# Optimization experiments

Measured on AMD Instinct MI355X. Metric: run time of the kernel, lower is better.

## Reference

```python
import jax, jax.numpy as jnp
import numpy as np

N, E, IN_DIM, HID, OUT, H = 50000, 800000, 128, 96, 96, 4
C1, C2 = HID // H, OUT // H
EPS = 1e-5

def _lin(key, out_f, in_f):
    kw, kb = jax.random.split(key)
    s = 1.0 / np.sqrt(in_f)
    W = jax.random.uniform(kw, (out_f, in_f), jnp.float32, -s, s)
    b = jax.random.uniform(kb, (out_f,), jnp.float32, -s, s)
    return W, b

def setup_inputs() -> dict:
    key = jax.random.key(0)
    ks = jax.random.split(key, 16)
    x = jax.random.normal(ks[0], (N, IN_DIM), jnp.float32)
    edge_index = jax.random.randint(ks[1], (2, E), 0, N, jnp.int64)
    Wq1, bq1 = _lin(ks[2], HID, IN_DIM)
    Wk1, bk1 = _lin(ks[3], HID, IN_DIM)
    Wv1, bv1 = _lin(ks[4], HID, IN_DIM)
    Ws1, bs1 = _lin(ks[5], HID, IN_DIM)
    Wb1 = _lin(ks[6], 1, 3 * HID)[0]
    Wq2, bq2 = _lin(ks[7], OUT, HID)
    Wk2, bk2 = _lin(ks[8], OUT, HID)
    Wv2, bv2 = _lin(ks[9], OUT, HID)
    Ws2, bs2 = _lin(ks[10], OUT, HID)
    Wb2 = _lin(ks[11], 1, 3 * OUT)[0]
    gamma = jnp.ones((OUT,), jnp.float32)
    beta = jnp.zeros((OUT,), jnp.float32)
    return dict(x=x, edge_index=edge_index, Wq1=Wq1, bq1=bq1, Wk1=Wk1, bk1=bk1,
                Wv1=Wv1, bv1=bv1, Ws1=Ws1, bs1=bs1, Wb1=Wb1,
                Wq2=Wq2, bq2=bq2, Wk2=Wk2, bk2=bk2, Wv2=Wv2, bv2=bv2,
                Ws2=Ws2, bs2=bs2, Wb2=Wb2, gamma=gamma, beta=beta)

def transformer_conv(x, src, dst, Wq, bq, Wk, bk, Wv, bv, Ws, bs, Wb, heads, ch):
    n = x.shape[0]
    q = (x @ Wq.T + bq).reshape(n, heads, ch)
    k = (x @ Wk.T + bk).reshape(n, heads, ch)
    v = (x @ Wv.T + bv).reshape(n, heads, ch)
    # per-edge attention logits [E, H]
    alpha = jnp.einsum('ehc,ehc->eh', q[dst], k[src]) / jnp.sqrt(jnp.float32(ch))
    amax = jax.ops.segment_max(alpha, dst, num_segments=n)
    a = jnp.exp(alpha - amax[dst])
    denom = jax.ops.segment_sum(a, dst, num_segments=n)
    a = a / denom[dst]
    msg = v[src] * a[:, :, None]                       # [E, H, C]
    out = jax.ops.segment_sum(msg, dst, num_segments=n).reshape(n, heads * ch)
    x_r = x @ Ws.T + bs                                # root/skip transform
    g = jax.nn.sigmoid(jnp.concatenate([out, x_r, out - x_r], -1) @ Wb.T)
    return g * x_r + (1.0 - g) * out

def reference(x, edge_index, Wq1, bq1, Wk1, bk1, Wv1, bv1, Ws1, bs1, Wb1,
              Wq2, bq2, Wk2, bk2, Wv2, bv2, Ws2, bs2, Wb2, gamma, beta):
    src, dst = edge_index[0], edge_index[1]
    h = transformer_conv(x, src, dst, Wq1, bq1, Wk1, bk1, Wv1, bv1, Ws1, bs1, Wb1, H, C1)
    h = jax.nn.gelu(h, approximate=False)
    h = transformer_conv(h, src, dst, Wq2, bq2, Wk2, bk2, Wv2, bv2, Ws2, bs2, Wb2, H, C2)
    mu = jnp.mean(h, axis=-1, keepdims=True)
    var = jnp.mean(jnp.square(h - mu), axis=-1, keepdims=True)
    return (h - mu) / jnp.sqrt(var + EPS) * gamma + beta
```

## Files before the change

### kernel.cpp

```cpp
#include <hip/hip_runtime.h>
#include <hip/hip_bf16.h>
#include <hip/hip_fp16.h>
#include <math.h>

constexpr int NN = 50000;
constexpr int EE = 800000;
constexpr int SCAN_NB = (NN + 255) / 256;

typedef short v8s __attribute__((ext_vector_type(8)));
typedef float v4f __attribute__((ext_vector_type(4)));

__device__ __forceinline__ short f2b(float f){
  __hip_bfloat16 h = __float2bfloat16(f);
  return *reinterpret_cast<short*>(&h);
}
__device__ __forceinline__ __half2 u2h2(unsigned int u){
  union { unsigned int u; __half2 h; } c; c.u = u; return c.h;
}

__global__ void hist_kernel(const int* __restrict__ ei, int* __restrict__ deg){
  int e = blockIdx.x * blockDim.x + threadIdx.x;
  if (e < EE) atomicAdd(&deg[ei[EE + e]], 1);
}

__global__ __launch_bounds__(256) void partial_sum_kernel(const int* __restrict__ deg,
                                                          int* __restrict__ psum){
  int b = blockIdx.x, tid = threadIdx.x, lane = tid & 63, wv = tid >> 6;
  int i = b * 256 + tid;
  int v = (i < NN) ? deg[i] : 0;
  #pragma unroll
  for (int m = 1; m < 64; m <<= 1) v += __shfl_xor(v, m);
  __shared__ int ws[4];
  if (lane == 0) ws[wv] = v;
  __syncthreads();
  if (tid == 0) psum[b] = ws[0] + ws[1] + ws[2] + ws[3];
}

__global__ __launch_bounds__(256) void scan_partials_kernel(int* __restrict__ psum){
  int tid = threadIdx.x, lane = tid & 63, wv = tid >> 6;
  int own = (tid < SCAN_NB) ? psum[tid] : 0;
  int v = own;
  #pragma unroll
  for (int off = 1; off < 64; off <<= 1){
    int t = __shfl_up(v, off);
    if (lane >= off) v += t;
  }
  __shared__ int ws[4];
  if (lane == 63) ws[wv] = v;
  __syncthreads();
  int add = 0;
  #pragma unroll
  for (int w = 0; w < 4; w++) if (w < wv) add += ws[w];
  if (tid < SCAN_NB) psum[tid] = v + add - own;
}

__global__ __launch_bounds__(256) void final_scan_kernel(const int* __restrict__ deg,
                                                         const int* __restrict__ psum,
                                                         int* __restrict__ row_ptr,
                                                         int* __restrict__ cursor){
  int b = blockIdx.x, tid = threadIdx.x, lane = tid & 63, wv = tid >> 6;
  int i = b * 256 + tid;
  int d = (i < NN) ? deg[i] : 0;
  int v = d;
  #pragma unroll
  for (int off = 1; off < 64; off <<= 1){
    int t = __shfl_up(v, off);
    if (lane >= off) v += t;
  }
  __shared__ int ws[4];
  if (lane == 63) ws[wv] = v;
  __syncthreads();
  int add = psum[b];
  #pragma unroll
  for (int w = 0; w < 4; w++) if (w < wv) add += ws[w];
  if (i < NN){
    row_ptr[i + 1] = add + v;
    cursor[i]      = add + v - d;
  }
  if (i == 0) row_ptr[0] = 0;
}

__global__ void fill_kernel(const int* __restrict__ ei, int* __restrict__ cursor,
                            unsigned short* __restrict__ col_src){
  int e = blockIdx.x * blockDim.x + threadIdx.x;
  if (e < EE){
    int src = ei[e], dst = ei[EE + e];
    int pos = atomicAdd(&cursor[dst], 1);
    col_src[pos] = (unsigned short)src;
  }
}

__global__ void pack_kernel(
    const float* __restrict__ Wq1, const float* __restrict__ bq1,
    const float* __restrict__ Wk1, const float* __restrict__ bk1,
    const float* __restrict__ Wv1, const float* __restrict__ bv1,
    const float* __restrict__ Ws1, const float* __restrict__ bs1,
    const float* __restrict__ Wq2, const float* __restrict__ bq2,
    const float* __restrict__ Wk2, const float* __restrict__ bk2,
    const float* __restrict__ Wv2, const float* __restrict__ bv2,
    const float* __restrict__ Ws2, const float* __restrict__ bs2,
    short* __restrict__ Wcat1, float* __restrict__ bcat1,
    short* __restrict__ Wcat2, float* __restrict__ bcat2){
  int c = blockIdx.x;
  int layer = c / 384, cc = c % 384;
  int which = cc / 96, r = cc % 96;
  const float* Wsel;
  const float* bsel;
  int K;
  short* Wd;
  float* bd;
  if (layer == 0){
    Wsel = which == 0 ? Wq1 : which == 1 ? Wk1 : which == 2 ? Wv1 : Ws1;
    bsel = which == 0 ? bq1 : which == 1 ? bk1 : which == 2 ? bv1 : bs1;
    K = 128; Wd = Wcat1; bd = bcat1;
  } else {
    Wsel = which == 0 ? Wq2 : which == 1 ? Wk2 : which == 2 ? Wv2 : Ws2;
    bsel = which == 0 ? bq2 : which == 1 ? bk2 : which == 2 ? bv2 : bs2;
    K = 96; Wd = Wcat2; bd = bcat2;
  }
  for (int k = threadIdx.x; k < K; k += blockDim.x)
    Wd[(size_t)cc * K + k] = f2b(Wsel[(size_t)r * K + k]);
  if (threadIdx.x == 0) bd[cc] = bsel[r];
}

template<int K, bool AF32>
__global__ __launch_bounds__(256) void gemm_kernel(const void* __restrict__ Ain,
                                                   const short* __restrict__ Wcat,
                                                   const float* __restrict__ bcat,
                                                   float* __restrict__ qs,
                                                   __half* __restrict__ kvb,
                                                   int M){
  constexpr int NK = K / 32;
  const int tid = threadIdx.x;
  const int lane = tid & 63, wid = tid >> 6;
  const int tile = blockIdx.x * 4 + wid;
  if (tile * 16 >= M) return;
  const int rt = tile * 16;
  const int fr = lane & 15, fk = lane >> 4;
  const int arow = rt + fr;

  v8s a[NK];
  if constexpr (AF32){
    const float* A = (const float*)Ain;
    #pragma unroll
    for (int ks = 0; ks < NK; ks++){
      const float* p = A + (size_t)arow * K + ks * 32 + fk * 8;
      float4 a0 = *(const float4*)p;
      float4 a1 = *(const float4*)(p + 4);
      v8s o;
      o[0] = f2b(a0.x); o[1] = f2b(a0.y); o[2] = f2b(a0.z); o[3] = f2b(a0.w);
      o[4] = f2b(a1.x); o[5] = f2b(a1.y); o[6] = f2b(a1.z); o[7] = f2b(a1.w);
      a[ks] = o;
    }
  } else {
    const short* A = (const short*)Ain;
    #pragma unroll
    for (int ks = 0; ks < NK; ks++)
      a[ks] = *(const v8s*)(A + (size_t)arow * K + ks * 32 + fk * 8);
  }

  #pragma unroll 4
  for (int p = 0; p < 24; p++){
    const int c0 = p * 16;
    const int gcol = c0 + fr;
    v4f acc = (v4f){0.f, 0.f, 0.f, 0.f};
    #pragma unroll
    for (int ks = 0; ks < NK; ks++){
      v8s b = *(const v8s*)(Wcat + (size_t)gcol * K + ks * 32 + fk * 8);
      acc = __builtin_amdgcn_mfma_f32_16x16x32_bf16(a[ks], b, acc, 0, 0, 0);
    }
    const float bias = bcat[gcol];
    if (c0 < 96){
      #pragma unroll
      for (int r = 0; r < 4; r++)
        qs[(size_t)(rt + fk * 4 + r) * 192 + gcol] = acc[r] + bias;
    } else if (c0 < 192){
      #pragma unroll
      for (int r = 0; r < 4; r++)
        kvb[(size_t)(rt + fk * 4 + r) * 192 + (gcol - 96)] = __float2half(acc[r] + bias);
    } else if (c0 < 288){
      #pragma unroll
      for (int r = 0; r < 4; r++)
        kvb[(size_t)(rt + fk * 4 + r) * 192 + 96 + (gcol - 192)] = __float2half(acc[r] + bias);
    } else {
      #pragma unroll
      for (int r = 0; r < 4; r++)
        qs[(size_t)(rt + fk * 4 + r) * 192 + 96 + (gcol - 288)] = acc[r] + bias;
    }
  }
}

__global__ __launch_bounds__(256) void attn_kernel(
    const float* __restrict__ qs, const __half* __restrict__ kv,
    const int* __restrict__ row_ptr, const unsigned short* __restrict__ col_src,
    const float* __restrict__ Wb, const float* __restrict__ gamma,
    const float* __restrict__ beta, float* __restrict__ outp,
    short* __restrict__ h1b, int mode){
  const int lane = threadIdx.x & 63;
  const int wid  = threadIdx.x >> 6;
  const int n = blockIdx.x * 4 + wid;
  if (n >= NN) return;
  const int h_a = lane & 3;
  const int g_a = lane >> 2;
  const int l_v = lane & 15;
  const int vg  = lane >> 4;
  const int h_v = l_v >> 2;

  __half2 qh[12];
  {
    const float* qrow = qs + (size_t)n * 192 + h_a * 24;
    #pragma unroll
    for (int i = 0; i < 12; i++)
      qh[i] = __floats2half2_rn(qrow[2 * i], qrow[2 * i + 1]);
  }
  const int rs = row_ptr[n], re = row_ptr[n + 1];
  float m = -INFINITY, s = 0.f;
  float acc[6] = {0.f, 0.f, 0.f, 0.f, 0.f, 0.f};

  for (int cb = rs; cb < re; cb += 16){
    const int cn = re - cb;
    int srcv = col_src[cb + min(g_a, cn - 1)];
    int sb[4];
    #pragma unroll
    for (int st = 0; st < 4; st++)
      sb[st] = __shfl(srcv, 4 * min(st * 4 + vg, cn - 1));
    unsigned int vd[4][3];
    #pragma unroll
    for (int st = 0; st < 4; st++){
      const unsigned int* vp =
        (const unsigned int*)((const char*)kv + (size_t)sb[st] * 384 + 192 + 12 * l_v);
      vd[st][0] = vp[0]; vd[st][1] = vp[1]; vd[st][2] = vp[2];
    }
    const uint4* kp = (const uint4*)((const char*)kv + (size_t)srcv * 384 + h_a * 48);
    uint4 u0 = kp[0], u1 = kp[1], u2 = kp[2];
    __half2 d0 = __floats2half2_rn(0.f, 0.f), d1 = d0;
    d0 = __hfma2(qh[0],  u2h2(u0.x), d0); d1 = __hfma2(qh[1],  u2h2(u0.y), d1);
    d0 = __hfma2(qh[2],  u2h2(u0.z), d0); d1 = __hfma2(qh[3],  u2h2(u0.w), d1);
    d0 = __hfma2(qh[4],  u2h2(u1.x), d0); d1 = __hfma2(qh[5],  u2h2(u1.y), d1);
    d0 = __hfma2(qh[6],  u2h2(u1.z), d0); d1 = __hfma2(qh[7],  u2h2(u1.w), d1);
    d0 = __hfma2(qh[8],  u2h2(u2.x), d0); d1 = __hfma2(qh[9],  u2h2(u2.y), d1);
    d0 = __hfma2(qh[10], u2h2(u2.z), d0); d1 = __hfma2(qh[11], u2h2(u2.w), d1);
    float dot = __low2float(d0) + __high2float(d0) + __low2float(d1) + __high2float(d1);
    float al = (g_a < cn) ? dot * 0.2041241452319315f : -INFINITY;

    float cm = al;
    cm = fmaxf(cm, __shfl_xor(cm, 4));
    cm = fmaxf(cm, __shfl_xor(cm, 8));
    cm = fmaxf(cm, __shfl_xor(cm, 16));
    cm = fmaxf(cm, __shfl_xor(cm, 32));
    float nm = fmaxf(m, cm);
    float r  = __expf(m - nm);
    float e  = __expf(al - nm);
    float cs = e;
    cs += __shfl_xor(cs, 4);
    cs += __shfl_xor(cs, 8);
    cs += __shfl_xor(cs, 16);
    cs += __shfl_xor(cs, 32);
    s = s * r + cs;
    m = nm;

    float rv = __shfl(r, h_v);
    __half2 ch0 = __floats2half2_rn(0.f, 0.f), ch1 = ch0, ch2 = ch0;
    #pragma unroll
    for (int st = 0; st < 4; st++){
      int eidx = st * 4 + vg;
      float w = __shfl(e, 4 * min(eidx, cn - 1) + h_v);
      if (eidx >= cn) w = 0.f;
      __half2 w2 = __float2half2_rn(w);
      ch0 = __hfma2(w2, u2h2(vd[st][0]), ch0);
      ch1 = __hfma2(w2, u2h2(vd[st][1]), ch1);
      ch2 = __hfma2(w2, u2h2(vd[st][2]), ch2);
    }
    acc[0] = fmaf(acc[0], rv, __low2float(ch0));
    acc[1] = fmaf(acc[1], rv, __high2float(ch0));
    acc[2] = fmaf(acc[2], rv, __low2float(ch1));
    acc[3] = fmaf(acc[3], rv, __high2float(ch1));
    acc[4] = fmaf(acc[4], rv, __low2float(ch2));
    acc[5] = fmaf(acc[5], rv, __high2float(ch2));
  }

  #pragma unroll
  for (int i = 0; i < 6; i++){
    acc[i] += __shfl_xor(acc[i], 16);
    acc[i] += __shfl_xor(acc[i], 32);
  }
  float sv  = __shfl(s, h_v);
  float inv = (re > rs) ? 1.0f / sv : 0.f;
  float o[6], xr[6];
  #pragma unroll
  for (int i = 0; i < 6; i++) o[i] = acc[i] * inv;
  const float* xrp = qs + (size_t)n * 192 + 96 + 6 * l_v;
  #pragma unroll
  for (int i = 0; i < 6; i++) xr[i] = xrp[i];

  float p = 0.f;
  #pragma unroll
  for (int i = 0; i < 6; i++){
    int f = 6 * l_v + i;
    p += Wb[f] * o[i] + Wb[96 + f] * xr[i] + Wb[192 + f] * (o[i] - xr[i]);
  }
  p += __shfl_xor(p, 1);
  p += __shfl_xor(p, 2);
  p += __shfl_xor(p, 4);
  p += __shfl_xor(p, 8);
  float g = 1.0f / (1.0f + __expf(-p));
  float y[6];
  #pragma unroll
  for (int i = 0; i < 6; i++) y[i] = g * xr[i] + (1.0f - g) * o[i];

  if (mode == 0){
    #pragma unroll
    for (int i = 0; i < 6; i++)
      y[i] = 0.5f * y[i] * (1.0f + erff(y[i] * 0.7071067811865475f));
    if (vg == 0){
      short* op = h1b + (size_t)n * 96 + 6 * l_v;
      #pragma unroll
      for (int i = 0; i < 6; i++) op[i] = f2b(y[i]);
    }
  } else {
    float ssum = y[0] + y[1] + y[2] + y[3] + y[4] + y[5];
    ssum += __shfl_xor(ssum, 1);
    ssum += __shfl_xor(ssum, 2);
    ssum += __shfl_xor(ssum, 4);
    ssum += __shfl_xor(ssum, 8);
    float mu = ssum * (1.0f / 96.0f);
    float vsum = 0.f;
    #pragma unroll
    for (int i = 0; i < 6; i++){ float d = y[i] - mu; vsum += d * d; }
    vsum += __shfl_xor(vsum, 1);
    vsum += __shfl_xor(vsum, 2);
    vsum += __shfl_xor(vsum, 4);
    vsum += __shfl_xor(vsum, 8);
    float invs = rsqrtf(vsum * (1.0f / 96.0f) + 1e-5f);
    if (vg == 0){
      float* op = outp + (size_t)n * 96 + 6 * l_v;
      #pragma unroll
      for (int i = 0; i < 6; i++){
        int f = 6 * l_v + i;
        op[i] = (y[i] - mu) * invs * gamma[f] + beta[f];
      }
    }
  }
}

extern "C" void kernel_launch(void* const* d_in, const int* in_sizes, int n_in,
                              void* d_out, int out_size, void* d_ws, size_t ws_size,
                              hipStream_t stream){
  const float* x    = (const float*)d_in[0];
  const int*   ei   = (const int*)d_in[1];
  const float* Wq1  = (const float*)d_in[2];
  const float* bq1  = (const float*)d_in[3];
  const float* Wk1  = (const float*)d_in[4];
  const float* bk1  = (const float*)d_in[5];
  const float* Wv1  = (const float*)d_in[6];
  const float* bv1  = (const float*)d_in[7];
  const float* Ws1  = (const float*)d_in[8];
  const float* bs1  = (const float*)d_in[9];
  const float* Wb1  = (const float*)d_in[10];
  const float* Wq2  = (const float*)d_in[11];
  const float* bq2  = (const float*)d_in[12];
  const float* Wk2  = (const float*)d_in[13];
  const float* bk2  = (const float*)d_in[14];
  const float* Wv2  = (const float*)d_in[15];
  const float* bv2  = (const float*)d_in[16];
  const float* Ws2  = (const float*)d_in[17];
  const float* bs2  = (const float*)d_in[18];
  const float* Wb2  = (const float*)d_in[19];
  const float* gamma = (const float*)d_in[20];
  const float* beta  = (const float*)d_in[21];
  float* out = (float*)d_out;

  char* ws = (char*)d_ws;
  size_t off = 0;
  auto take = [&](size_t b) -> void* {
    void* p = ws + off;
    off += (b + 255) & ~(size_t)255;
    return p;
  };
  float* qs            = (float*)take((size_t)NN * 192 * 4);
  __half* kvb          = (__half*)take((size_t)NN * 192 * 2);
  short* h1b           = (short*)take((size_t)NN * 96 * 2);
  short* Wcat1         = (short*)take((size_t)384 * 128 * 2);
  short* Wcat2         = (short*)take((size_t)384 * 96 * 2);
  float* bcat1         = (float*)take(384 * 4);
  float* bcat2         = (float*)take(384 * 4);
  int* deg             = (int*)take((size_t)NN * 4);
  int* cursor          = (int*)take((size_t)NN * 4);
  int* row_ptr         = (int*)take((size_t)(NN + 1) * 4);
  unsigned short* col_src = (unsigned short*)take((size_t)EE * 2);
  int* psum            = (int*)take((size_t)SCAN_NB * 4);

  hipMemsetAsync(deg, 0, (size_t)NN * 4, stream);
  hist_kernel<<<(EE + 255) / 256, 256, 0, stream>>>(ei, deg);
  partial_sum_kernel<<<SCAN_NB, 256, 0, stream>>>(deg, psum);
  scan_partials_kernel<<<1, 256, 0, stream>>>(psum);
  final_scan_kernel<<<SCAN_NB, 256, 0, stream>>>(deg, psum, row_ptr, cursor);
  fill_kernel<<<(EE + 255) / 256, 256, 0, stream>>>(ei, cursor, col_src);

  pack_kernel<<<768, 128, 0, stream>>>(Wq1, bq1, Wk1, bk1, Wv1, bv1, Ws1, bs1,
                                       Wq2, bq2, Wk2, bk2, Wv2, bv2, Ws2, bs2,
                                       Wcat1, bcat1, Wcat2, bcat2);

  const int gemm_grid = ((NN + 15) / 16 + 3) / 4;
  gemm_kernel<128, true><<<gemm_grid, 256, 0, stream>>>(x, Wcat1, bcat1, qs, kvb, NN);
  attn_kernel<<<(NN + 3) / 4, 256, 0, stream>>>(qs, kvb, row_ptr, col_src, Wb1,
                                                nullptr, nullptr, nullptr, h1b, 0);
  gemm_kernel<96, false><<<gemm_grid, 256, 0, stream>>>(h1b, Wcat2, bcat2, qs, kvb, NN);
  attn_kernel<<<(NN + 3) / 4, 256, 0, stream>>>(qs, kvb, row_ptr, col_src, Wb2,
                                                gamma, beta, out, nullptr, 1);
}
```

Measured before the change: 291.0 us.

## Pad degree/cursor counters, store q and skip in fp16, prefetch next edge indices

Degree and cursor counters are spread out to one per 64 bytes so the atomics in the histogram and fill kernels do not contend on shared cache lines. The q/skip projection buffer is now written in fp16 instead of fp32, which halves its traffic, and the attention kernel loads it with vector reads. The edge loop also prefetches the next chunk's source indices. The trade-offs are a 16x larger memset and scan footprint for the counters, plus lower precision on the skip path.

```diff
diff --git a/kernel.cpp b/kernel.cpp
--- a/kernel.cpp
+++ b/kernel.cpp
@@ -20,14 +20,14 @@
 
 __global__ void hist_kernel(const int* __restrict__ ei, int* __restrict__ deg){
   int e = blockIdx.x * blockDim.x + threadIdx.x;
-  if (e < EE) atomicAdd(&deg[ei[EE + e]], 1);
+  if (e < EE) atomicAdd(&deg[ei[EE + e] << 4], 1);
 }
 
 __global__ __launch_bounds__(256) void partial_sum_kernel(const int* __restrict__ deg,
                                                           int* __restrict__ psum){
   int b = blockIdx.x, tid = threadIdx.x, lane = tid & 63, wv = tid >> 6;
   int i = b * 256 + tid;
-  int v = (i < NN) ? deg[i] : 0;
+  int v = (i < NN) ? deg[i << 4] : 0;
   #pragma unroll
   for (int m = 1; m < 64; m <<= 1) v += __shfl_xor(v, m);
   __shared__ int ws[4];
@@ -60,7 +60,7 @@
                                                          int* __restrict__ cursor){
   int b = blockIdx.x, tid = threadIdx.x, lane = tid & 63, wv = tid >> 6;
   int i = b * 256 + tid;
-  int d = (i < NN) ? deg[i] : 0;
+  int d = (i < NN) ? deg[i << 4] : 0;
   int v = d;
   #pragma unroll
   for (int off = 1; off < 64; off <<= 1){
@@ -75,7 +75,7 @@
   for (int w = 0; w < 4; w++) if (w < wv) add += ws[w];
   if (i < NN){
     row_ptr[i + 1] = add + v;
-    cursor[i]      = add + v - d;
+    cursor[i << 4] = add + v - d;
   }
   if (i == 0) row_ptr[0] = 0;
 }
@@ -85,7 +85,7 @@
   int e = blockIdx.x * blockDim.x + threadIdx.x;
   if (e < EE){
     int src = ei[e], dst = ei[EE + e];
-    int pos = atomicAdd(&cursor[dst], 1);
+    int pos = atomicAdd(&cursor[dst << 4], 1);
     col_src[pos] = (unsigned short)src;
   }
 }
@@ -127,7 +127,7 @@
 __global__ __launch_bounds__(256) void gemm_kernel(const void* __restrict__ Ain,
                                                    const short* __restrict__ Wcat,
                                                    const float* __restrict__ bcat,
-                                                   float* __restrict__ qs,
+                                                   __half* __restrict__ qsh,
                                                    __half* __restrict__ kvb,
                                                    int M){
   constexpr int NK = K / 32;
@@ -173,7 +173,7 @@
     if (c0 < 96){
       #pragma unroll
       for (int r = 0; r < 4; r++)
-        qs[(size_t)(rt + fk * 4 + r) * 192 + gcol] = acc[r] + bias;
+        qsh[(size_t)(rt + fk * 4 + r) * 192 + gcol] = __float2half(acc[r] + bias);
     } else if (c0 < 192){
       #pragma unroll
       for (int r = 0; r < 4; r++)
@@ -185,13 +185,13 @@
     } else {
       #pragma unroll
       for (int r = 0; r < 4; r++)
-        qs[(size_t)(rt + fk * 4 + r) * 192 + 96 + (gcol - 288)] = acc[r] + bias;
+        qsh[(size_t)(rt + fk * 4 + r) * 192 + 96 + (gcol - 288)] = __float2half(acc[r] + bias);
     }
   }
 }
 
 __global__ __launch_bounds__(256) void attn_kernel(
-    const float* __restrict__ qs, const __half* __restrict__ kv,
+    const __half* __restrict__ qs, const __half* __restrict__ kv,
     const int* __restrict__ row_ptr, const unsigned short* __restrict__ col_src,
     const float* __restrict__ Wb, const float* __restrict__ gamma,
     const float* __restrict__ beta, float* __restrict__ outp,
@@ -205,78 +205,86 @@
   const int l_v = lane & 15;
   const int vg  = lane >> 4;
   const int h_v = l_v >> 2;
+  const char* kvc = (const char*)kv;
+  const char* qsc = (const char*)qs;
 
   __half2 qh[12];
   {
-    const float* qrow = qs + (size_t)n * 192 + h_a * 24;
-    #pragma unroll
-    for (int i = 0; i < 12; i++)
-      qh[i] = __floats2half2_rn(qrow[2 * i], qrow[2 * i + 1]);
+    const uint4* qp = (const uint4*)(qsc + (size_t)n * 384 + h_a * 48);
+    uint4 a0 = qp[0], a1 = qp[1], a2 = qp[2];
+    qh[0] = u2h2(a0.x); qh[1] = u2h2(a0.y); qh[2]  = u2h2(a0.z); qh[3]  = u2h2(a0.w);
+    qh[4] = u2h2(a1.x); qh[5] = u2h2(a1.y); qh[6]  = u2h2(a1.z); qh[7]  = u2h2(a1.w);
+    qh[8] = u2h2(a2.x); qh[9] = u2h2(a2.y); qh[10] = u2h2(a2.z); qh[11] = u2h2(a2.w);
   }
   const int rs = row_ptr[n], re = row_ptr[n + 1];
   float m = -INFINITY, s = 0.f;
   float acc[6] = {0.f, 0.f, 0.f, 0.f, 0.f, 0.f};
 
-  for (int cb = rs; cb < re; cb += 16){
-    const int cn = re - cb;
-    int srcv = col_src[cb + min(g_a, cn - 1)];
-    int sb[4];
-    #pragma unroll
-    for (int st = 0; st < 4; st++)
-      sb[st] = __shfl(srcv, 4 * min(st * 4 + vg, cn - 1));
-    unsigned int vd[4][3];
-    #pragma unroll
-    for (int st = 0; st < 4; st++){
-      const unsigned int* vp =
-        (const unsigned int*)((const char*)kv + (size_t)sb[st] * 384 + 192 + 12 * l_v);
-      vd[st][0] = vp[0]; vd[st][1] = vp[1]; vd[st][2] = vp[2];
-    }
-    const uint4* kp = (const uint4*)((const char*)kv + (size_t)srcv * 384 + h_a * 48);
-    uint4 u0 = kp[0], u1 = kp[1], u2 = kp[2];
-    __half2 d0 = __floats2half2_rn(0.f, 0.f), d1 = d0;
-    d0 = __hfma2(qh[0],  u2h2(u0.x), d0); d1 = __hfma2(qh[1],  u2h2(u0.y), d1);
-    d0 = __hfma2(qh[2],  u2h2(u0.z), d0); d1 = __hfma2(qh[3],  u2h2(u0.w), d1);
-    d0 = __hfma2(qh[4],  u2h2(u1.x), d0); d1 = __hfma2(qh[5],  u2h2(u1.y), d1);
-    d0 = __hfma2(qh[6],  u2h2(u1.z), d0); d1 = __hfma2(qh[7],  u2h2(u1.w), d1);
-    d0 = __hfma2(qh[8],  u2h2(u2.x), d0); d1 = __hfma2(qh[9],  u2h2(u2.y), d1);
-    d0 = __hfma2(qh[10], u2h2(u2.z), d0); d1 = __hfma2(qh[11], u2h2(u2.w), d1);
-    float dot = __low2float(d0) + __high2float(d0) + __low2float(d1) + __high2float(d1);
-    float al = (g_a < cn) ? dot * 0.2041241452319315f : -INFINITY;
-
-    float cm = al;
-    cm = fmaxf(cm, __shfl_xor(cm, 4));
-    cm = fmaxf(cm, __shfl_xor(cm, 8));
-    cm = fmaxf(cm, __shfl_xor(cm, 16));
-    cm = fmaxf(cm, __shfl_xor(cm, 32));
-    float nm = fmaxf(m, cm);
-    float r  = __expf(m - nm);
-    float e  = __expf(al - nm);
-    float cs = e;
-    cs += __shfl_xor(cs, 4);
-    cs += __shfl_xor(cs, 8);
-    cs += __shfl_xor(cs, 16);
-    cs += __shfl_xor(cs, 32);
-    s = s * r + cs;
-    m = nm;
-
-    float rv = __shfl(r, h_v);
-    __half2 ch0 = __floats2half2_rn(0.f, 0.f), ch1 = ch0, ch2 = ch0;
-    #pragma unroll
-    for (int st = 0; st < 4; st++){
-      int eidx = st * 4 + vg;
-      float w = __shfl(e, 4 * min(eidx, cn - 1) + h_v);
-      if (eidx >= cn) w = 0.f;
-      __half2 w2 = __float2half2_rn(w);
-      ch0 = __hfma2(w2, u2h2(vd[st][0]), ch0);
-      ch1 = __hfma2(w2, u2h2(vd[st][1]), ch1);
-      ch2 = __hfma2(w2, u2h2(vd[st][2]), ch2);
-    }
-    acc[0] = fmaf(acc[0], rv, __low2float(ch0));
-    acc[1] = fmaf(acc[1], rv, __high2float(ch0));
-    acc[2] = fmaf(acc[2], rv, __low2float(ch1));
-    acc[3] = fmaf(acc[3], rv, __high2float(ch1));
-    acc[4] = fmaf(acc[4], rv, __low2float(ch2));
-    acc[5] = fmaf(acc[5], rv, __high2float(ch2));
+  if (re > rs){
+    int srcv = col_src[rs + min(g_a, re - rs - 1)];
+    for (int cb = rs; cb < re; cb += 16){
+      const int cn = re - cb;
+      const int srcv_cur = srcv;
+      if (cb + 16 < re)
+        srcv = col_src[cb + 16 + min(g_a, re - cb - 17)];
+      int sb[4];
+      #pragma unroll
+      for (int st = 0; st < 4; st++)
+        sb[st] = __shfl(srcv_cur, 4 * min(st * 4 + vg, cn - 1));
+      unsigned int vd[4][3];
+      #pragma unroll
+      for (int st = 0; st < 4; st++){
+        const unsigned int* vp =
+          (const unsigned int*)(kvc + (size_t)sb[st] * 384 + 192 + 12 * l_v);
+        vd[st][0] = vp[0]; vd[st][1] = vp[1]; vd[st][2] = vp[2];
+      }
+      const uint4* kp = (const uint4*)(kvc + (size_t)srcv_cur * 384 + h_a * 48);
+      uint4 u0 = kp[0], u1 = kp[1], u2 = kp[2];
+      __half2 d0 = __floats2half2_rn(0.f, 0.f), d1 = d0;
+      d0 = __hfma2(qh[0],  u2h2(u0.x), d0); d1 = __hfma2(qh[1],  u2h2(u0.y), d1);
+      d0 = __hfma2(qh[2],  u2h2(u0.z), d0); d1 = __hfma2(qh[3],  u2h2(u0.w), d1);
+      d0 = __hfma2(qh[4],  u2h2(u1.x), d0); d1 = __hfma2(qh[5],  u2h2(u1.y), d1);
+      d0 = __hfma2(qh[6],  u2h2(u1.z), d0); d1 = __hfma2(qh[7],  u2h2(u1.w), d1);
+      d0 = __hfma2(qh[8],  u2h2(u2.x), d0); d1 = __hfma2(qh[9],  u2h2(u2.y), d1);
+      d0 = __hfma2(qh[10], u2h2(u2.z), d0); d1 = __hfma2(qh[11], u2h2(u2.w), d1);
+      float dot = __low2float(d0) + __high2float(d0) + __low2float(d1) + __high2float(d1);
+      float al = (g_a < cn) ? dot * 0.2041241452319315f : -INFINITY;
+
+      float cm = al;
+      cm = fmaxf(cm, __shfl_xor(cm, 4));
+      cm = fmaxf(cm, __shfl_xor(cm, 8));
+      cm = fmaxf(cm, __shfl_xor(cm, 16));
+      cm = fmaxf(cm, __shfl_xor(cm, 32));
+      float nm = fmaxf(m, cm);
+      float r  = __expf(m - nm);
+      float e  = __expf(al - nm);
+      float cs = e;
+      cs += __shfl_xor(cs, 4);
+      cs += __shfl_xor(cs, 8);
+      cs += __shfl_xor(cs, 16);
+      cs += __shfl_xor(cs, 32);
+      s = s * r + cs;
+      m = nm;
+
+      float rv = __shfl(r, h_v);
+      __half2 ch0 = __floats2half2_rn(0.f, 0.f), ch1 = ch0, ch2 = ch0;
+      #pragma unroll
+      for (int st = 0; st < 4; st++){
+        int eidx = st * 4 + vg;
+        float w = __shfl(e, 4 * min(eidx, cn - 1) + h_v);
+        if (eidx >= cn) w = 0.f;
+        __half2 w2 = __float2half2_rn(w);
+        ch0 = __hfma2(w2, u2h2(vd[st][0]), ch0);
+        ch1 = __hfma2(w2, u2h2(vd[st][1]), ch1);
+        ch2 = __hfma2(w2, u2h2(vd[st][2]), ch2);
+      }
+      acc[0] = fmaf(acc[0], rv, __low2float(ch0));
+      acc[1] = fmaf(acc[1], rv, __high2float(ch0));
+      acc[2] = fmaf(acc[2], rv, __low2float(ch1));
+      acc[3] = fmaf(acc[3], rv, __high2float(ch1));
+      acc[4] = fmaf(acc[4], rv, __low2float(ch2));
+      acc[5] = fmaf(acc[5], rv, __high2float(ch2));
+    }
   }
 
   #pragma unroll
@@ -289,9 +297,13 @@
   float o[6], xr[6];
   #pragma unroll
   for (int i = 0; i < 6; i++) o[i] = acc[i] * inv;
-  const float* xrp = qs + (size_t)n * 192 + 96 + 6 * l_v;
-  #pragma unroll
-  for (int i = 0; i < 6; i++) xr[i] = xrp[i];
+  {
+    const unsigned int* xp = (const unsigned int*)(qsc + (size_t)n * 384 + 192 + 12 * l_v);
+    unsigned int x0 = xp[0], x1 = xp[1], x2 = xp[2];
+    xr[0] = __low2float(u2h2(x0)); xr[1] = __high2float(u2h2(x0));
+    xr[2] = __low2float(u2h2(x1)); xr[3] = __high2float(u2h2(x1));
+    xr[4] = __low2float(u2h2(x2)); xr[5] = __high2float(u2h2(x2));
+  }
 
   float p = 0.f;
   #pragma unroll
@@ -377,20 +389,20 @@
     off += (b + 255) & ~(size_t)255;
     return p;
   };
-  float* qs            = (float*)take((size_t)NN * 192 * 4);
+  __half* qs           = (__half*)take((size_t)NN * 192 * 2);
   __half* kvb          = (__half*)take((size_t)NN * 192 * 2);
   short* h1b           = (short*)take((size_t)NN * 96 * 2);
   short* Wcat1         = (short*)take((size_t)384 * 128 * 2);
   short* Wcat2         = (short*)take((size_t)384 * 96 * 2);
   float* bcat1         = (float*)take(384 * 4);
   float* bcat2         = (float*)take(384 * 4);
-  int* deg             = (int*)take((size_t)NN * 4);
-  int* cursor          = (int*)take((size_t)NN * 4);
+  int* deg             = (int*)take((size_t)NN * 64);
+  int* cursor          = (int*)take((size_t)NN * 64);
   int* row_ptr         = (int*)take((size_t)(NN + 1) * 4);
   unsigned short* col_src = (unsigned short*)take((size_t)EE * 2);
   int* psum            = (int*)take((size_t)SCAN_NB * 4);
 
-  hipMemsetAsync(deg, 0, (size_t)NN * 4, stream);
+  hipMemsetAsync(deg, 0, (size_t)NN * 64, stream);
   hist_kernel<<<(EE + 255) / 256, 256, 0, stream>>>(ei, deg);
   partial_sum_kernel<<<SCAN_NB, 256, 0, stream>>>(deg, psum);
   scan_partials_kernel<<<1, 256, 0, stream>>>(psum);
```

Measured after the change: 289.7 us. Within noise of the previous version (-0.4%).
